# Kernel tuning notes

Measured on AMD Instinct MI355X. Metric: run time of the kernel, lower is better.

The kernel has to match this reference:

```python
import jax, jax.numpy as jnp
import numpy as np

B, N, M, C1, C2 = 4, 8192, 2048, 128, 256
H1, H2 = 256, 128  # mlp = [C2+C1, 256, 128]
EPS_DIST = 1e-8
EPS_BN = 1e-5
K = 3


def setup_inputs() -> dict:
    key = jax.random.key(0)
    ks = jax.random.split(key, 6)
    return {
        "unknown": jax.random.normal(ks[0], (B, N, 3), dtype=jnp.float32),
        "known": jax.random.normal(ks[1], (B, M, 3), dtype=jnp.float32),
        "unknow_feats": jax.random.normal(ks[2], (B, C1, N), dtype=jnp.float32),
        "known_feats": jax.random.normal(ks[3], (B, C2, M), dtype=jnp.float32),
        "W1": jax.random.normal(ks[4], (H1, C1 + C2), dtype=jnp.float32) * 0.05,
        "g1": jnp.ones((H1,), jnp.float32),
        "b1": jnp.zeros((H1,), jnp.float32),
        "W2": jax.random.normal(ks[5], (H2, H1), dtype=jnp.float32) * 0.05,
        "g2": jnp.ones((H2,), jnp.float32),
        "b2": jnp.zeros((H2,), jnp.float32),
    }


def _bn_relu(x, g, b):
    # training-mode BatchNorm over (batch, spatial) axes for (B, C, N) tensor
    mean = jnp.mean(x, axis=(0, 2), keepdims=True)
    var = jnp.var(x, axis=(0, 2), keepdims=True)
    y = (x - mean) * jax.lax.rsqrt(var + EPS_BN) * g[None, :, None] + b[None, :, None]
    return jax.nn.relu(y)


def reference(unknown, known, unknow_feats, known_feats, W1, g1, b1, W2, g2, b2):
    # 3-NN: squared euclidean distances (B, N, M) via expansion (avoids B,N,M,3 temp)
    d2 = (
        jnp.sum(unknown * unknown, axis=-1)[:, :, None]
        + jnp.sum(known * known, axis=-1)[:, None, :]
        - 2.0 * jnp.einsum("bnc,bmc->bnm", unknown, known)
    )
    neg_d, idx = jax.lax.top_k(-d2, K)  # smallest-K squared dists
    dist = -neg_d  # (B, N, K), squared distances (pytorch3d knn_points convention)
    recip = 1.0 / (dist + EPS_DIST)
    weight = recip / jnp.sum(recip, axis=2, keepdims=True)  # (B, N, K)

    kf = jnp.swapaxes(known_feats, 1, 2)  # (B, M, C2)
    grouped = jax.vmap(lambda f, i: f[i])(kf, idx)  # (B, N, K, C2)
    interp = jnp.einsum("bnkc,bnk->bcn", grouped, weight)  # (B, C2, N)

    x = jnp.concatenate([interp, unknow_feats], axis=1)  # (B, C2+C1, N)
    x = _bn_relu(jnp.einsum("oc,bcn->bon", W1, x), g1, b1)
    x = _bn_relu(jnp.einsum("oc,bcn->bon", W2, x), g2, b2)
    return x  # (B, H2, N)
```

## Files before the change

### kernel.cpp

```cpp
#include <hip/hip_runtime.h>
#include <hip/hip_bf16.h>
#include <cstdint>
#include <cstddef>

typedef unsigned short u16;
typedef __attribute__((ext_vector_type(8))) short bf16x8;
typedef __attribute__((ext_vector_type(4))) float f32x4;

constexpr int Bn = 4;
constexpr int Nq = 8192;
constexpr int Mk = 2048;
constexpr int C1c = 128;
constexpr int C2c = 256;
constexpr int H1c = 256;
constexpr int H2c = 128;

__device__ __forceinline__ float bf2f(u16 u) {
    union { uint32_t i; float f; } v;
    v.i = (uint32_t)u << 16;
    return v.f;
}
__device__ __forceinline__ u16 f2bf(float f) {
    const uint32_t x = __float_as_uint(f);
    return (u16)((x + 0x7FFFu + ((x >> 16) & 1u)) >> 16);
}
__device__ __forceinline__ uint32_t cvtpk(float lo, float hi) {
    uint32_t r;
    asm("v_cvt_pk_bf16_f32 %0, %1, %2" : "=v"(r) : "v"(lo), "v"(hi));
    return r;
}

__global__ __launch_bounds__(256) void knn_prep_kernel(
    const float* __restrict__ W1, const float* __restrict__ W2,
    u16* __restrict__ W1b, u16* __restrict__ W2b,
    const float* __restrict__ KF, u16* __restrict__ Ptb,
    const float* __restrict__ UF, u16* __restrict__ UFt,
    const float* __restrict__ unknown, const float* __restrict__ known,
    int* __restrict__ idx_out, float* __restrict__ w_out)
{
    __shared__ __align__(16) char smem[32768];
    const int bid = blockIdx.x;
    const int t = threadIdx.x;

    if (bid < 1024) {
        float4* kp = (float4*)smem;
        const int b = bid >> 8;
        const int n0 = (bid & 255) * 32;

        const float* kb = known + (size_t)b * Mk * 3;
        for (int i = t; i < Mk; i += 256) {
            const float x = kb[i * 3 + 0], y = kb[i * 3 + 1], z = kb[i * 3 + 2];
            kp[i] = make_float4(x, y, z, fmaf(x, x, fmaf(y, y, z * z)));
        }
        __syncthreads();

        const int q = n0 + (t >> 3);
        const int s = t & 7;
        const float* u = unknown + ((size_t)b * Nq + q) * 3;
        const float ux = u[0], uy = u[1], uz = u[2];
        const float nux = -2.0f * ux, nuy = -2.0f * uy, nuz = -2.0f * uz;
        const float uu = fmaf(ux, ux, fmaf(uy, uy, uz * uz));

        float d0 = 1e30f, d1 = 1e30f, d2 = 1e30f;
        int i0 = 0, i1 = 0, i2 = 0;

        auto ins = [&](float d, int i) {
            const bool c0 = d < d0, c1 = d < d1, c2 = d < d2;
            const float nd0 = fminf(d0, d);
            const float nd1 = __builtin_amdgcn_fmed3f(d0, d, d1);
            const float nd2 = __builtin_amdgcn_fmed3f(d1, d, d2);
            i2 = c1 ? i1 : (c2 ? i : i2);
            i1 = c0 ? i0 : (c1 ? i : i1);
            i0 = c0 ? i : i0;
            d0 = nd0; d1 = nd1; d2 = nd2;
        };

        #pragma unroll 8
        for (int it = 0; it < Mk / 8; ++it) {
            const int m = it * 8 + s;
            const float4 p = kp[m];
            const float d = fmaf(nux, p.x, fmaf(nuy, p.y, fmaf(nuz, p.z, p.w)));
            ins(d, m);
        }
        #pragma unroll
        for (int off = 1; off <= 4; off <<= 1) {
            const float e0 = __shfl_xor(d0, off), e1 = __shfl_xor(d1, off), e2 = __shfl_xor(d2, off);
            const int j0 = __shfl_xor(i0, off), j1 = __shfl_xor(i1, off), j2 = __shfl_xor(i2, off);
            ins(e0, j0);
            ins(e1, j1);
            ins(e2, j2);
        }
        if (s == 0) {
            const float f0 = d0 + uu, f1 = d1 + uu, f2 = d2 + uu;
            const float r0 = 1.0f / (f0 + 1e-8f);
            const float r1 = 1.0f / (f1 + 1e-8f);
            const float r2 = 1.0f / (f2 + 1e-8f);
            const float inv = 1.0f / (r0 + r1 + r2);
            const size_t base = ((size_t)b * Nq + q) * 3;
            idx_out[base + 0] = i0;
            idx_out[base + 1] = i1;
            idx_out[base + 2] = i2;
            w_out[base + 0] = r0 * inv;
            w_out[base + 1] = r1 * inv;
            w_out[base + 2] = r2 * inv;
        }
    } else if (bid < 1152) {
        const int cb = bid - 1024;
        const float* X = (cb < 96) ? W1 : W2;
        u16* Y = (cb < 96) ? W1b : W2b;
        const int i = ((cb < 96) ? cb : (cb - 96)) * 256 + t;
        const float4 v = *(const float4*)&X[(size_t)i * 4];
        ushort4 o;
        o.x = f2bf(v.x); o.y = f2bf(v.y); o.z = f2bf(v.z); o.w = f2bf(v.w);
        *(ushort4*)&Y[(size_t)i * 4] = o;
    } else if (bid < 1664) {
        u16* As = (u16*)smem;
        u16* Bs = (u16*)(smem + 5120);
        const int f = bid - 1152;
        const int b = f >> 7;
        const int rem = f & 127;
        const int m0 = (rem >> 2) * 64;
        const int h0 = (rem & 3) * 64;
        const float* KFb = KF + (size_t)b * C2c * Mk;
        const int l = t & 63, wv = t >> 6;
        const int wr = wv >> 1, wc = wv & 1;

        f32x4 acc[2][2];
        const f32x4 z = {0.0f, 0.0f, 0.0f, 0.0f};
        acc[0][0] = z; acc[0][1] = z; acc[1][0] = z; acc[1][1] = z;

        const int cA = t >> 3;
        const int mcA = (t & 7) * 8;
        const int hB = t >> 2;
        const int khB = (t & 3) * 8;

        for (int kt = 0; kt < 8; ++kt) {
            const int kc = kt * 32;
            {
                const float* src = &KFb[(size_t)(kc + cA) * Mk + m0 + mcA];
                const float4 v0 = *(const float4*)&src[0];
                const float4 v1 = *(const float4*)&src[4];
                As[(mcA + 0) * 40 + cA] = f2bf(v0.x);
                As[(mcA + 1) * 40 + cA] = f2bf(v0.y);
                As[(mcA + 2) * 40 + cA] = f2bf(v0.z);
                As[(mcA + 3) * 40 + cA] = f2bf(v0.w);
                As[(mcA + 4) * 40 + cA] = f2bf(v1.x);
                As[(mcA + 5) * 40 + cA] = f2bf(v1.y);
                As[(mcA + 6) * 40 + cA] = f2bf(v1.z);
                As[(mcA + 7) * 40 + cA] = f2bf(v1.w);
            }
            {
                const float* src = &W1[(size_t)(h0 + hB) * 384 + kc + khB];
                const float4 v0 = *(const float4*)&src[0];
                const float4 v1 = *(const float4*)&src[4];
                u16 o[8] = {f2bf(v0.x), f2bf(v0.y), f2bf(v0.z), f2bf(v0.w),
                            f2bf(v1.x), f2bf(v1.y), f2bf(v1.z), f2bf(v1.w)};
                *(uint4*)&Bs[hB * 40 + khB] = *(const uint4*)o;
            }
            __syncthreads();
            bf16x8 af[2], bf[2];
            #pragma unroll
            for (int ff = 0; ff < 2; ++ff) {
                af[ff] = *(const bf16x8*)&As[(wr * 32 + ff * 16 + (l & 15)) * 40 + (l >> 4) * 8];
                bf[ff] = *(const bf16x8*)&Bs[(wc * 32 + ff * 16 + (l & 15)) * 40 + (l >> 4) * 8];
            }
            #pragma unroll
            for (int i = 0; i < 2; ++i)
                #pragma unroll
                for (int j = 0; j < 2; ++j)
                    acc[i][j] = __builtin_amdgcn_mfma_f32_16x16x32_bf16(af[i], bf[j], acc[i][j], 0, 0, 0);
            __syncthreads();
        }

        u16* Pb = Ptb + (size_t)b * Mk * 256;
        const int cb = l & 15, rg = (l >> 4) * 4;
        #pragma unroll
        for (int i = 0; i < 2; ++i) {
            #pragma unroll
            for (int r = 0; r < 4; ++r) {
                const int row = m0 + wr * 32 + i * 16 + rg + r;
                #pragma unroll
                for (int j = 0; j < 2; ++j)
                    Pb[(size_t)row * 256 + h0 + wc * 32 + j * 16 + cb] = f2bf(acc[i][j][r]);
            }
        }
    } else {
        const int f = bid - 1664;
        const int b = f >> 8, rem = f & 255;
        const int m0 = (rem >> 1) * 64, c0 = (rem & 1) * 64;
        const float* X = UF + (size_t)b * C1c * Nq;
        u16* Y = UFt + (size_t)b * Nq * C1c;
        float (*T)[65] = (float(*)[65])smem;
        const int m4 = (t & 15) * 4, cr = t >> 4;
        #pragma unroll
        for (int i = 0; i < 4; ++i) {
            const float4 v = *(const float4*)&X[(size_t)(c0 + cr + i * 16) * Nq + m0 + m4];
            T[cr + i * 16][m4 + 0] = v.x;
            T[cr + i * 16][m4 + 1] = v.y;
            T[cr + i * 16][m4 + 2] = v.z;
            T[cr + i * 16][m4 + 3] = v.w;
        }
        __syncthreads();
        const int c4 = (t & 15) * 4, mr = t >> 4;
        #pragma unroll
        for (int i = 0; i < 4; ++i) {
            const int m = mr + i * 16;
            ushort4 o;
            o.x = f2bf(T[c4 + 0][m]);
            o.y = f2bf(T[c4 + 1][m]);
            o.z = f2bf(T[c4 + 2][m]);
            o.w = f2bf(T[c4 + 3][m]);
            *(ushort4*)&Y[(size_t)(m0 + m) * C1c + c0 + c4] = o;
        }
    }
}

__global__ __launch_bounds__(256) void mfma_gemm2(
    const u16* __restrict__ A, const u16* __restrict__ Bt,
    u16* __restrict__ Cout, const u16* __restrict__ Ptb,
    const int* __restrict__ idx, const float* __restrict__ wgt,
    float* __restrict__ partS, float* __restrict__ partQ)
{
    __shared__ __align__(16) char smem[16384];
    __shared__ float redS[4][128], redQ[4][128];
    u16* As = (u16*)smem;
    u16* Bs = (u16*)(smem + 8192);
    float (*Ytmp)[128] = (float(*)[128])smem;

    const int b = blockIdx.z;
    const int m0 = blockIdx.x * 128, n0 = blockIdx.y * 128;
    const int t = threadIdx.x;
    const int l = t & 63, wv = t >> 6;
    const int wr = wv >> 1, wc = wv & 1;

    const u16* Ab = A + (size_t)b * Nq * C1c;
    const int rA0 = t >> 2, rA1 = (t + 256) >> 2;
    const int ko = (t & 3) * 8;

    f32x4 acc[4][4];
    const f32x4 z = {0.0f, 0.0f, 0.0f, 0.0f};
    #pragma unroll
    for (int i = 0; i < 4; ++i)
        #pragma unroll
        for (int j = 0; j < 4; ++j) acc[i][j] = z;

    uint4 a0 = *(const uint4*)&Ab[(size_t)(m0 + rA0) * C1c + ko];
    uint4 a1 = *(const uint4*)&Ab[(size_t)(m0 + rA1) * C1c + ko];
    uint4 b0 = *(const uint4*)&Bt[(size_t)(n0 + rA0) * 384 + ko];
    uint4 b1 = *(const uint4*)&Bt[(size_t)(n0 + rA1) * 384 + ko];

    for (int kt = 0; kt < C1c / 32; ++kt) {
        *(uint4*)&As[t * 8] = a0;
        *(uint4*)&As[(t + 256) * 8] = a1;
        *(uint4*)&Bs[t * 8] = b0;
        *(uint4*)&Bs[(t + 256) * 8] = b1;
        __syncthreads();
        if (kt + 1 < C1c / 32) {
            const int k0 = (kt + 1) * 32;
            a0 = *(const uint4*)&Ab[(size_t)(m0 + rA0) * C1c + k0 + ko];
            a1 = *(const uint4*)&Ab[(size_t)(m0 + rA1) * C1c + k0 + ko];
            b0 = *(const uint4*)&Bt[(size_t)(n0 + rA0) * 384 + k0 + ko];
            b1 = *(const uint4*)&Bt[(size_t)(n0 + rA1) * 384 + k0 + ko];
        }
        bf16x8 af[4], bf[4];
        #pragma unroll
        for (int f = 0; f < 4; ++f) {
            af[f] = *(const bf16x8*)&As[(wr * 64 + f * 16 + (l & 15)) * 32 + (l >> 4) * 8];
            bf[f] = *(const bf16x8*)&Bs[(wc * 64 + f * 16 + (l & 15)) * 32 + (l >> 4) * 8];
        }
        #pragma unroll
        for (int i = 0; i < 4; ++i)
            #pragma unroll
            for (int j = 0; j < 4; ++j)
                acc[i][j] = __builtin_amdgcn_mfma_f32_16x16x32_bf16(af[i], bf[j], acc[i][j], 0, 0, 0);
        __syncthreads();
    }

    const int cb = l & 15;
    const int rg = (l >> 4) * 4;
    const int colblk = t & 15;
    const int rowblk = t >> 4;
    float s8[8] = {0, 0, 0, 0, 0, 0, 0, 0}, q8[8] = {0, 0, 0, 0, 0, 0, 0, 0};
    const u16* Pb = Ptb + (size_t)b * Mk * 256;

    for (int q = 0; q < 4; ++q) {
        __syncthreads();
        if (wr == (q >> 1)) {
            #pragma unroll
            for (int ii = 0; ii < 2; ++ii) {
                const int i = (q & 1) * 2 + ii;
                #pragma unroll
                for (int r = 0; r < 4; ++r) {
                    const int Rq = ii * 16 + rg + r;
                    #pragma unroll
                    for (int j = 0; j < 4; ++j)
                        Ytmp[Rq][wc * 64 + j * 16 + cb] = acc[i][j][r];
                }
            }
        }
        __syncthreads();
        #pragma unroll
        for (int rr = 0; rr < 2; ++rr) {
            const int Rq = rowblk * 2 + rr;
            const int R = m0 + q * 32 + Rq;
            const size_t ib = ((size_t)b * Nq + R) * 3;
            const int j0 = idx[ib], j1 = idx[ib + 1], j2 = idx[ib + 2];
            const float w0 = wgt[ib], w1 = wgt[ib + 1], w2 = wgt[ib + 2];
            const int c8 = colblk * 8;
            const int Cc0 = n0 + c8;
            const float* yrow = &Ytmp[Rq][c8];
            const float4 y0 = *(const float4*)&yrow[0];
            const float4 y1v = *(const float4*)&yrow[4];
            const uint4 p0 = *(const uint4*)&Pb[(size_t)j0 * 256 + Cc0];
            const uint4 p1 = *(const uint4*)&Pb[(size_t)j1 * 256 + Cc0];
            const uint4 p2 = *(const uint4*)&Pb[(size_t)j2 * 256 + Cc0];
            const u16* pp0 = (const u16*)&p0;
            const u16* pp1 = (const u16*)&p1;
            const u16* pp2 = (const u16*)&p2;
            const float* ya = (const float*)&y0;
            const float* yb = (const float*)&y1v;
            float v[8];
            #pragma unroll
            for (int c = 0; c < 8; ++c) {
                const float a = (c < 4) ? ya[c] : yb[c - 4];
                const float vv = a + w0 * bf2f(pp0[c]) + w1 * bf2f(pp1[c]) + w2 * bf2f(pp2[c]);
                v[c] = vv;
                s8[c] += vv;
                q8[c] += vv * vv;
            }
            uint4 o;
            uint32_t* po = (uint32_t*)&o;
            po[0] = cvtpk(v[0], v[1]);
            po[1] = cvtpk(v[2], v[3]);
            po[2] = cvtpk(v[4], v[5]);
            po[3] = cvtpk(v[6], v[7]);
            *(uint4*)&Cout[(size_t)b * Nq * 256 + (size_t)R * 256 + Cc0] = o;
        }
    }

    #pragma unroll
    for (int c = 0; c < 8; ++c) {
        s8[c] += __shfl_xor(s8[c], 16);
        s8[c] += __shfl_xor(s8[c], 32);
        q8[c] += __shfl_xor(q8[c], 16);
        q8[c] += __shfl_xor(q8[c], 32);
    }
    if (l < 16) {
        #pragma unroll
        for (int c = 0; c < 8; ++c) {
            redS[wv][l * 8 + c] = s8[c];
            redQ[wv][l * 8 + c] = q8[c];
        }
    }
    __syncthreads();
    if (t < 128) {
        const float S = redS[0][t] + redS[1][t] + redS[2][t] + redS[3][t];
        const float Q = redQ[0][t] + redQ[1][t] + redQ[2][t] + redQ[3][t];
        const int pblk = blockIdx.z * gridDim.x + blockIdx.x;
        partS[(size_t)pblk * 256 + blockIdx.y * 128 + t] = S;
        partQ[(size_t)pblk * 256 + blockIdx.y * 128 + t] = Q;
    }
}

__global__ __launch_bounds__(256) void bn1_finalize_mb(
    const float* __restrict__ pS, const float* __restrict__ pQ,
    const float* __restrict__ g, const float* __restrict__ beta,
    float* __restrict__ scale, float* __restrict__ bias)
{
    __shared__ float rs[256], rq[256];
    const int cc = threadIdx.x & 15;
    const int sl = threadIdx.x >> 4;
    const int ch = blockIdx.x * 16 + cc;
    float s = 0.0f, q = 0.0f;
    for (int i = sl; i < 256; i += 16) {
        s += pS[(size_t)i * 256 + ch];
        q += pQ[(size_t)i * 256 + ch];
    }
    rs[threadIdx.x] = s;
    rq[threadIdx.x] = q;
    __syncthreads();
    if (sl == 0) {
        for (int k = 1; k < 16; ++k) {
            s += rs[k * 16 + cc];
            q += rq[k * 16 + cc];
        }
        const float cnt = (float)(Bn * Nq);
        const float mean = s / cnt;
        const float var = q / cnt - mean * mean;
        const float rv = rsqrtf(var + 1e-5f);
        const float sc = g[ch] * rv;
        scale[ch] = sc;
        bias[ch] = beta[ch] - mean * sc;
    }
}

__device__ __forceinline__ uint4 bnx(uint4 x, const float* scs, const float* bis, int k) {
    const u16* p = (const u16*)&x;
    const float4 s0 = *(const float4*)&scs[k];
    const float4 s1 = *(const float4*)&scs[k + 4];
    const float4 b0 = *(const float4*)&bis[k];
    const float4 b1 = *(const float4*)&bis[k + 4];
    const float* sa = (const float*)&s0;
    const float* sb = (const float*)&s1;
    const float* ba = (const float*)&b0;
    const float* bb = (const float*)&b1;
    uint4 o;
    uint32_t* po = (uint32_t*)&o;
    #pragma unroll
    for (int w2 = 0; w2 < 2; ++w2) {
        const float a0 = fmaxf(0.0f, fmaf(bf2f(p[2 * w2 + 0]), sa[2 * w2 + 0], ba[2 * w2 + 0]));
        const float a1 = fmaxf(0.0f, fmaf(bf2f(p[2 * w2 + 1]), sa[2 * w2 + 1], ba[2 * w2 + 1]));
        po[w2] = cvtpk(a0, a1);
    }
    #pragma unroll
    for (int w2 = 0; w2 < 2; ++w2) {
        const float a0 = fmaxf(0.0f, fmaf(bf2f(p[4 + 2 * w2 + 0]), sb[2 * w2 + 0], bb[2 * w2 + 0]));
        const float a1 = fmaxf(0.0f, fmaf(bf2f(p[4 + 2 * w2 + 1]), sb[2 * w2 + 1], bb[2 * w2 + 1]));
        po[2 + w2] = cvtpk(a0, a1);
    }
    return o;
}

__global__ __launch_bounds__(256) void mfma_gemm3(
    const u16* __restrict__ W2b,
    const u16* __restrict__ Y,
    u16* __restrict__ y2b,
    const float* __restrict__ bn_s, const float* __restrict__ bn_b,
    float* __restrict__ partS, float* __restrict__ partQ)
{
    __shared__ u16 As[2048];
    __shared__ u16 Bs[4096];
    __shared__ float scs[256], bis[256];
    __shared__ float sS[2][64], sQ[2][64];

    const int b = blockIdx.z;
    const int m0 = blockIdx.x * 64;
    const int n0 = blockIdx.y * 128;
    const int t = threadIdx.x;
    const int l = t & 63, wv = t >> 6;
    const int wr = wv >> 1, wc = wv & 1;

    scs[t] = bn_s[t];
    bis[t] = bn_b[t];

    const u16* Yb = Y + (size_t)b * Nq * 256;
    const int rA = t >> 2;
    const int rB1 = (t + 256) >> 2;
    const int ko = (t & 3) * 8;

    f32x4 acc[2][4];
    const f32x4 z = {0.0f, 0.0f, 0.0f, 0.0f};
    #pragma unroll
    for (int i = 0; i < 2; ++i)
        #pragma unroll
        for (int j = 0; j < 4; ++j) acc[i][j] = z;

    uint4 a0 = *(const uint4*)&W2b[(size_t)(m0 + rA) * 256 + ko];
    uint4 b0 = *(const uint4*)&Yb[(size_t)(n0 + rA) * 256 + ko];
    uint4 b1 = *(const uint4*)&Yb[(size_t)(n0 + rB1) * 256 + ko];
    __syncthreads();

    for (int kt = 0; kt < 8; ++kt) {
        const int k = kt * 32 + ko;
        *(uint4*)&As[t * 8] = a0;
        *(uint4*)&Bs[t * 8] = bnx(b0, scs, bis, k);
        *(uint4*)&Bs[(t + 256) * 8] = bnx(b1, scs, bis, k);
        __syncthreads();
        if (kt + 1 < 8) {
            const int k0 = (kt + 1) * 32;
            a0 = *(const uint4*)&W2b[(size_t)(m0 + rA) * 256 + k0 + ko];
            b0 = *(const uint4*)&Yb[(size_t)(n0 + rA) * 256 + k0 + ko];
            b1 = *(const uint4*)&Yb[(size_t)(n0 + rB1) * 256 + k0 + ko];
        }
        bf16x8 af[2], bf[4];
        #pragma unroll
        for (int f = 0; f < 2; ++f)
            af[f] = *(const bf16x8*)&As[(wr * 32 + f * 16 + (l & 15)) * 32 + (l >> 4) * 8];
        #pragma unroll
        for (int f = 0; f < 4; ++f)
            bf[f] = *(const bf16x8*)&Bs[(wc * 64 + f * 16 + (l & 15)) * 32 + (l >> 4) * 8];
        #pragma unroll
        for (int i = 0; i < 2; ++i)
            #pragma unroll
            for (int j = 0; j < 4; ++j)
                acc[i][j] = __builtin_amdgcn_mfma_f32_16x16x32_bf16(af[i], bf[j], acc[i][j], 0, 0, 0);
        __syncthreads();
    }

    const int cb = l & 15;
    const int rg = (l >> 4) * 4;
    u16* ob = y2b + (size_t)b * H2c * Nq;
    #pragma unroll
    for (int i = 0; i < 2; ++i) {
        #pragma unroll
        for (int r = 0; r < 4; ++r) {
            const int Rl = wr * 32 + i * 16 + rg + r;
            #pragma unroll
            for (int j = 0; j < 4; ++j) {
                const int Cc = n0 + wc * 64 + j * 16 + cb;
                ob[(size_t)(m0 + Rl) * Nq + Cc] = f2bf(acc[i][j][r]);
            }
            float s = acc[i][0][r] + acc[i][1][r] + acc[i][2][r] + acc[i][3][r];
            float q = acc[i][0][r] * acc[i][0][r] + acc[i][1][r] * acc[i][1][r] +
                      acc[i][2][r] * acc[i][2][r] + acc[i][3][r] * acc[i][3][r];
            s += __shfl_xor(s, 1); s += __shfl_xor(s, 2);
            s += __shfl_xor(s, 4); s += __shfl_xor(s, 8);
            q += __shfl_xor(q, 1); q += __shfl_xor(q, 2);
            q += __shfl_xor(q, 4); q += __shfl_xor(q, 8);
            if ((l & 15) == 0) {
                sS[wc][Rl] = s;
                sQ[wc][Rl] = q;
            }
        }
    }
    __syncthreads();
    if (t < 64) {
        const float S = sS[0][t] + sS[1][t];
        const float Q = sQ[0][t] + sQ[1][t];
        const int p = blockIdx.z * gridDim.y + blockIdx.y;
        partS[(size_t)p * 128 + m0 + t] = S;
        partQ[(size_t)p * 128 + m0 + t] = Q;
    }
}

__global__ __launch_bounds__(256) void bn2_finalize_mb(
    const float* __restrict__ pS, const float* __restrict__ pQ,
    const float* __restrict__ g, const float* __restrict__ beta,
    float* __restrict__ scale, float* __restrict__ bias)
{
    __shared__ float rs[256], rq[256];
    const int cc = threadIdx.x & 15;
    const int sl = threadIdx.x >> 4;
    const int ch = blockIdx.x * 16 + cc;
    float s = 0.0f, q = 0.0f;
    for (int i = sl; i < 256; i += 16) {
        s += pS[(size_t)i * 128 + ch];
        q += pQ[(size_t)i * 128 + ch];
    }
    rs[threadIdx.x] = s;
    rq[threadIdx.x] = q;
    __syncthreads();
    if (sl == 0) {
        for (int k = 1; k < 16; ++k) {
            s += rs[k * 16 + cc];
            q += rq[k * 16 + cc];
        }
        const float cnt = (float)(Bn * Nq);
        const float mean = s / cnt;
        const float var = q / cnt - mean * mean;
        const float rv = rsqrtf(var + 1e-5f);
        const float sc = g[ch] * rv;
        scale[ch] = sc;
        bias[ch] = beta[ch] - mean * sc;
    }
}

__global__ __launch_bounds__(256) void bn2_apply_simple(
    const u16* __restrict__ y2b, float* __restrict__ out,
    const float* __restrict__ scale, const float* __restrict__ bias)
{
    const size_t base = (size_t)blockIdx.x * 2048;
    const int c = (int)((base / Nq) % H2c);
    const float sc = scale[c], bi = bias[c];
    const size_t i = base + threadIdx.x * 8;
    const uint4 v = *(const uint4*)&y2b[i];
    const u16* pv = (const u16*)&v;
    float4 o0, o1;
    o0.x = fmaxf(0.0f, fmaf(bf2f(pv[0]), sc, bi));
    o0.y = fmaxf(0.0f, fmaf(bf2f(pv[1]), sc, bi));
    o0.z = fmaxf(0.0f, fmaf(bf2f(pv[2]), sc, bi));
    o0.w = fmaxf(0.0f, fmaf(bf2f(pv[3]), sc, bi));
    o1.x = fmaxf(0.0f, fmaf(bf2f(pv[4]), sc, bi));
    o1.y = fmaxf(0.0f, fmaf(bf2f(pv[5]), sc, bi));
    o1.z = fmaxf(0.0f, fmaf(bf2f(pv[6]), sc, bi));
    o1.w = fmaxf(0.0f, fmaf(bf2f(pv[7]), sc, bi));
    *(float4*)&out[i] = o0;
    *(float4*)&out[i + 4] = o1;
}

extern "C" void kernel_launch(void* const* d_in, const int* in_sizes, int n_in,
                              void* d_out, int out_size, void* d_ws, size_t ws_size,
                              hipStream_t stream) {
    const float* unknown = (const float*)d_in[0];
    const float* known = (const float*)d_in[1];
    const float* unknow_feats = (const float*)d_in[2];
    const float* known_feats = (const float*)d_in[3];
    const float* W1 = (const float*)d_in[4];
    const float* g1 = (const float*)d_in[5];
    const float* b1 = (const float*)d_in[6];
    const float* W2 = (const float*)d_in[7];
    const float* g2 = (const float*)d_in[8];
    const float* b2 = (const float*)d_in[9];
    float* out = (float*)d_out;

    char* w = (char*)d_ws;
    u16* UFt = (u16*)w; w += (size_t)Bn * Nq * C1c * 2;
    u16* W1b = (u16*)w; w += (size_t)H1c * 384 * 2;
    u16* W2b = (u16*)w; w += (size_t)H2c * H1c * 2;
    u16* Ptb = (u16*)w; w += (size_t)Bn * Mk * H1c * 2;
    u16* y1b = (u16*)w; w += (size_t)Bn * Nq * H1c * 2;
    u16* y2b = (u16*)w; w += (size_t)Bn * H2c * Nq * 2;
    int* idx = (int*)w; w += (size_t)Bn * Nq * 3 * 4;
    float* wgt = (float*)w; w += (size_t)Bn * Nq * 3 * 4;
    float* pS1 = (float*)w; w += (size_t)256 * 256 * 4;
    float* pQ1 = (float*)w; w += (size_t)256 * 256 * 4;
    float* pS2 = (float*)w; w += (size_t)256 * 128 * 4;
    float* pQ2 = (float*)w; w += (size_t)256 * 128 * 4;
    float* scale1 = (float*)w; w += 1024;
    float* bias1 = (float*)w; w += 1024;
    float* scale2 = (float*)w; w += 1024;
    float* bias2 = (float*)w; w += 1024;

    knn_prep_kernel<<<2688, 256, 0, stream>>>(W1, W2, W1b, W2b,
                                              known_feats, Ptb, unknow_feats, UFt,
                                              unknown, known, idx, wgt);

    mfma_gemm2<<<dim3(Nq / 128, H1c / 128, Bn), 256, 0, stream>>>(
        UFt, W1b + C2c, y1b, Ptb, idx, wgt, pS1, pQ1);

    bn1_finalize_mb<<<16, 256, 0, stream>>>(pS1, pQ1, g1, b1, scale1, bias1);

    mfma_gemm3<<<dim3(2, Nq / 128, Bn), 256, 0, stream>>>(
        W2b, y1b, y2b, scale1, bias1, pS2, pQ2);

    bn2_finalize_mb<<<8, 256, 0, stream>>>(pS2, pQ2, g2, b2, scale2, bias2);

    bn2_apply_simple<<<(Bn * H2c * Nq) / 2048, 256, 0, stream>>>(y2b, out, scale2, bias2);
}
```

Baseline: 91.24 us.

## Fuse unknown-feature transpose and bf16 conversion into first GEMM A-tile load

Drops the separate transpose/convert section of the prep kernel that wrote a bf16 transposed copy of unknow_feats to workspace. The first GEMM now reads fp32 features directly in their (C, N) layout, converts them to bf16 and transposes them into a padded shared-memory tile with stride 40. This removes a full write and re-read of an 8 MB intermediate and 1024 prep blocks. In exchange, each unknow_feats tile is read twice, once per H1 block, and converted redundantly, and the scalar transposed LDS stores may cause bank conflicts.

After: 92.48 us. About the same (+1.4%).

```diff
diff --git a/kernel.cpp b/kernel.cpp
--- a/kernel.cpp
+++ b/kernel.cpp
@@ -34,7 +34,6 @@
     const float* __restrict__ W1, const float* __restrict__ W2,
     u16* __restrict__ W1b, u16* __restrict__ W2b,
     const float* __restrict__ KF, u16* __restrict__ Ptb,
-    const float* __restrict__ UF, u16* __restrict__ UFt,
     const float* __restrict__ unknown, const float* __restrict__ known,
     int* __restrict__ idx_out, float* __restrict__ w_out)
 {
@@ -113,7 +112,7 @@
         ushort4 o;
         o.x = f2bf(v.x); o.y = f2bf(v.y); o.z = f2bf(v.z); o.w = f2bf(v.w);
         *(ushort4*)&Y[(size_t)i * 4] = o;
-    } else if (bid < 1664) {
+    } else {
         u16* As = (u16*)smem;
         u16* Bs = (u16*)(smem + 5120);
         const int f = bid - 1152;
@@ -184,47 +183,21 @@
                     Pb[(size_t)row * 256 + h0 + wc * 32 + j * 16 + cb] = f2bf(acc[i][j][r]);
             }
         }
-    } else {
-        const int f = bid - 1664;
-        const int b = f >> 8, rem = f & 255;
-        const int m0 = (rem >> 1) * 64, c0 = (rem & 1) * 64;
-        const float* X = UF + (size_t)b * C1c * Nq;
-        u16* Y = UFt + (size_t)b * Nq * C1c;
-        float (*T)[65] = (float(*)[65])smem;
-        const int m4 = (t & 15) * 4, cr = t >> 4;
-        #pragma unroll
-        for (int i = 0; i < 4; ++i) {
-            const float4 v = *(const float4*)&X[(size_t)(c0 + cr + i * 16) * Nq + m0 + m4];
-            T[cr + i * 16][m4 + 0] = v.x;
-            T[cr + i * 16][m4 + 1] = v.y;
-            T[cr + i * 16][m4 + 2] = v.z;
-            T[cr + i * 16][m4 + 3] = v.w;
-        }
-        __syncthreads();
-        const int c4 = (t & 15) * 4, mr = t >> 4;
-        #pragma unroll
-        for (int i = 0; i < 4; ++i) {
-            const int m = mr + i * 16;
-            ushort4 o;
-            o.x = f2bf(T[c4 + 0][m]);
-            o.y = f2bf(T[c4 + 1][m]);
-            o.z = f2bf(T[c4 + 2][m]);
-            o.w = f2bf(T[c4 + 3][m]);
-            *(ushort4*)&Y[(size_t)(m0 + m) * C1c + c0 + c4] = o;
-        }
     }
 }
 
 __global__ __launch_bounds__(256) void mfma_gemm2(
-    const u16* __restrict__ A, const u16* __restrict__ Bt,
-    u16* __restrict__ Cout, const u16* __restrict__ Ptb,
+    const float* __restrict__ UF,
+    const u16* __restrict__ Bt,
+    u16* __restrict__ Cout,
+    const u16* __restrict__ Ptb,
     const int* __restrict__ idx, const float* __restrict__ wgt,
     float* __restrict__ partS, float* __restrict__ partQ)
 {
-    __shared__ __align__(16) char smem[16384];
+    __shared__ __align__(16) char smem[18944];
     __shared__ float redS[4][128], redQ[4][128];
     u16* As = (u16*)smem;
-    u16* Bs = (u16*)(smem + 8192);
+    u16* Bs = (u16*)(smem + 10240);
     float (*Ytmp)[128] = (float(*)[128])smem;
 
     const int b = blockIdx.z;
@@ -233,9 +206,13 @@
     const int l = t & 63, wv = t >> 6;
     const int wr = wv >> 1, wc = wv & 1;
 
-    const u16* Ab = A + (size_t)b * Nq * C1c;
-    const int rA0 = t >> 2, rA1 = (t + 256) >> 2;
-    const int ko = (t & 3) * 8;
+    const float* UFb = UF + (size_t)b * C1c * Nq;
+    const int cA = t >> 3;
+    const int nA = (t & 7) * 16;
+    const int rB = t >> 1;
+    const int kB = (t & 1) * 16;
+    const int rB0 = t >> 2, rB1v = (t + 256) >> 2;
+    const int koB = (t & 3) * 8;
 
     f32x4 acc[4][4];
     const f32x4 z = {0.0f, 0.0f, 0.0f, 0.0f};
@@ -244,28 +221,37 @@
         #pragma unroll
         for (int j = 0; j < 4; ++j) acc[i][j] = z;
 
-    uint4 a0 = *(const uint4*)&Ab[(size_t)(m0 + rA0) * C1c + ko];
-    uint4 a1 = *(const uint4*)&Ab[(size_t)(m0 + rA1) * C1c + ko];
-    uint4 b0 = *(const uint4*)&Bt[(size_t)(n0 + rA0) * 384 + ko];
-    uint4 b1 = *(const uint4*)&Bt[(size_t)(n0 + rA1) * 384 + ko];
+    float4 ua[4];
+    #pragma unroll
+    for (int i = 0; i < 4; ++i)
+        ua[i] = *(const float4*)&UFb[(size_t)cA * Nq + m0 + nA + i * 4];
+    uint4 b0 = *(const uint4*)&Bt[(size_t)(n0 + rB0) * 384 + koB];
+    uint4 b1 = *(const uint4*)&Bt[(size_t)(n0 + rB1v) * 384 + koB];
 
     for (int kt = 0; kt < C1c / 32; ++kt) {
-        *(uint4*)&As[t * 8] = a0;
-        *(uint4*)&As[(t + 256) * 8] = a1;
-        *(uint4*)&Bs[t * 8] = b0;
-        *(uint4*)&Bs[(t + 256) * 8] = b1;
+        #pragma unroll
+        for (int i = 0; i < 4; ++i) {
+            const float* pv = (const float*)&ua[i];
+            As[(nA + i * 4 + 0) * 40 + cA] = f2bf(pv[0]);
+            As[(nA + i * 4 + 1) * 40 + cA] = f2bf(pv[1]);
+            As[(nA + i * 4 + 2) * 40 + cA] = f2bf(pv[2]);
+            As[(nA + i * 4 + 3) * 40 + cA] = f2bf(pv[3]);
+        }
+        *(uint4*)&Bs[(size_t)rB0 * 32 + koB] = b0;
+        *(uint4*)&Bs[(size_t)rB1v * 32 + koB] = b1;
         __syncthreads();
         if (kt + 1 < C1c / 32) {
             const int k0 = (kt + 1) * 32;
-            a0 = *(const uint4*)&Ab[(size_t)(m0 + rA0) * C1c + k0 + ko];
-            a1 = *(const uint4*)&Ab[(size_t)(m0 + rA1) * C1c + k0 + ko];
-            b0 = *(const uint4*)&Bt[(size_t)(n0 + rA0) * 384 + k0 + ko];
-            b1 = *(const uint4*)&Bt[(size_t)(n0 + rA1) * 384 + k0 + ko];
+            #pragma unroll
+            for (int i = 0; i < 4; ++i)
+                ua[i] = *(const float4*)&UFb[(size_t)(k0 + cA) * Nq + m0 + nA + i * 4];
+            b0 = *(const uint4*)&Bt[(size_t)(n0 + rB0) * 384 + k0 + koB];
+            b1 = *(const uint4*)&Bt[(size_t)(n0 + rB1v) * 384 + k0 + koB];
         }
         bf16x8 af[4], bf[4];
         #pragma unroll
         for (int f = 0; f < 4; ++f) {
-            af[f] = *(const bf16x8*)&As[(wr * 64 + f * 16 + (l & 15)) * 32 + (l >> 4) * 8];
+            af[f] = *(const bf16x8*)&As[(wr * 64 + f * 16 + (l & 15)) * 40 + (l >> 4) * 8];
             bf[f] = *(const bf16x8*)&Bs[(wc * 64 + f * 16 + (l & 15)) * 32 + (l >> 4) * 8];
         }
         #pragma unroll
@@ -594,7 +580,6 @@
     float* out = (float*)d_out;
 
     char* w = (char*)d_ws;
-    u16* UFt = (u16*)w; w += (size_t)Bn * Nq * C1c * 2;
     u16* W1b = (u16*)w; w += (size_t)H1c * 384 * 2;
     u16* W2b = (u16*)w; w += (size_t)H2c * H1c * 2;
     u16* Ptb = (u16*)w; w += (size_t)Bn * Mk * H1c * 2;
@@ -611,12 +596,12 @@
     float* scale2 = (float*)w; w += 1024;
     float* bias2 = (float*)w; w += 1024;
 
-    knn_prep_kernel<<<2688, 256, 0, stream>>>(W1, W2, W1b, W2b,
-                                              known_feats, Ptb, unknow_feats, UFt,
+    knn_prep_kernel<<<1664, 256, 0, stream>>>(W1, W2, W1b, W2b,
+                                              known_feats, Ptb,
                                               unknown, known, idx, wgt);
 
     mfma_gemm2<<<dim3(Nq / 128, H1c / 128, Bn), 256, 0, stream>>>(
-        UFt, W1b + C2c, y1b, Ptb, idx, wgt, pS1, pQ1);
+        unknow_feats, W1b + C2c, y1b, Ptb, idx, wgt, pS1, pQ1);
 
     bn1_finalize_mb<<<16, 256, 0, stream>>>(pS1, pQ1, g1, b1, scale1, bias1);
 
```
